# Kernel optimization log

Measured on AMD Instinct MI355X. Metric: run time of the kernel, lower is better.

Reference implementation:

```python
import jax, jax.numpy as jnp
import numpy as np
from jax import lax

B, N, D = 64, 499, 256          # batch, nodes(=seq_len), emb_size
NUM_P, NUM_Q, NUM_C = 10000, 2000, 10


def _seg_softmax(e, dst, n):
    # e: [E,H] edge scores, segment softmax over destination node
    m = jax.ops.segment_max(e, dst, num_segments=n)
    ex = jnp.exp(e - m[dst])
    s = jax.ops.segment_sum(ex, dst, num_segments=n)
    return ex / s[dst]


def gat_conv(x, src, dst, W, a_src, a_dst, b, concat):
    # x: [B,n,Fin], W: [Fin,H*Fo], a_src/a_dst: [H,Fo], b: [H*Fo] or [Fo]
    Bn, n, _ = x.shape
    H, Fo = a_src.shape
    h = (x @ W).reshape(Bn, n, H, Fo)
    es = jnp.einsum('bnhf,hf->bnh', h, a_src)
    ed = jnp.einsum('bnhf,hf->bnh', h, a_dst)
    e = jax.nn.leaky_relu(es[:, src] + ed[:, dst], 0.2)   # [B,E,H]
    alpha = jax.vmap(lambda eb: _seg_softmax(eb, dst, n))(e)
    msg = alpha[..., None] * h[:, src]                    # [B,E,H,Fo]
    out = jax.vmap(lambda mb: jax.ops.segment_sum(mb, dst, num_segments=n))(msg)
    out = out.reshape(Bn, n, H * Fo) if concat else out.mean(axis=2)
    return out + b


def lstm(xs, W_ih, W_hh, b_ih, b_hh):
    # xs: [B,S,I]; torch gate order i,f,g,o
    Bn = xs.shape[0]
    Hd = W_hh.shape[1]

    def step(carry, xt):
        h, c = carry
        g = xt @ W_ih.T + b_ih + h @ W_hh.T + b_hh
        i, f, gg, o = jnp.split(g, 4, axis=-1)
        c = jax.nn.sigmoid(f) * c + jax.nn.sigmoid(i) * jnp.tanh(gg)
        h = jax.nn.sigmoid(o) * jnp.tanh(c)
        return (h, c), h

    init = (jnp.zeros((Bn, Hd), xs.dtype), jnp.zeros((Bn, Hd), xs.dtype))
    _, hs = lax.scan(step, init, xs.transpose(1, 0, 2))
    return hs.transpose(1, 0, 2)


def _edges():
    # genr_edge_index(true_length-1=498): chain over nodes 0..497, then
    # PyG GATConv removes self-loops and adds them back for all 499 nodes.
    L = N - 1
    src, dst = [], []
    for i in range(L):
        for j in (i - 1, i + 1):
            if 0 <= j < L:
                src.append(i)
                dst.append(j)
    src += list(range(N))
    dst += list(range(N))
    return np.array(src, np.int32), np.array(dst, np.int32)


def setup_inputs() -> dict:
    key = jax.random.key(0)
    ks = jax.random.split(key, 30)
    f32 = jnp.float32

    def nrm(k, shape, s=0.05):
        return jax.random.normal(k, shape, dtype=f32) * s

    src, dst = _edges()
    inp = {
        'true_length': jnp.full((B,), N, dtype=jnp.int32),
        'p': jax.random.randint(ks[0], (B, N), 0, NUM_P + 1, dtype=jnp.int32),
        'q': jax.random.randint(ks[1], (B, N), 0, NUM_Q + 1, dtype=jnp.int32),
        'r': jax.random.randint(ks[2], (B, N), 0, 2, dtype=jnp.int32),
        'aff': jax.random.randint(ks[3], (B, N), 0, NUM_C + 1, dtype=jnp.int32),
        'q_next': jax.random.randint(ks[4], (B, N), 0, NUM_Q + 1, dtype=jnp.int32),
        'p_next': jax.random.randint(ks[5], (B, N), 0, NUM_P + 1, dtype=jnp.int32),
        'src': jnp.asarray(src),
        'dst': jnp.asarray(dst),
        'emb_p': nrm(ks[6], (NUM_P + 1, D), 1.0),
        'emb_q': nrm(ks[7], (NUM_Q + 1, D), 1.0),
        'emb_r': nrm(ks[8], (2, D), 1.0),
        'emb_aff': nrm(ks[9], (NUM_C + 1, D), 1.0),
        'W_affcat': nrm(ks[10], (2 * D, D)),
        'b_affcat': nrm(ks[11], (D,)),
        'W_g1': nrm(ks[12], (D, 8 * 128)),
        'a_src1': nrm(ks[13], (8, 128)),
        'a_dst1': nrm(ks[14], (8, 128)),
        'b_g1': nrm(ks[15], (8 * 128,)),
        'W_g2': nrm(ks[16], (8 * 128, D)),
        'a_src2': nrm(ks[17], (1, D)),
        'a_dst2': nrm(ks[18], (1, D)),
        'b_g2': nrm(ks[19], (D,)),
        'W_ih': nrm(ks[20], (4 * D, 4 * D)),
        'W_hh': nrm(ks[21], (4 * D, D)),
        'b_ih': nrm(ks[22], (4 * D,)),
        'b_hh': nrm(ks[23], (4 * D,)),
        'W_out': nrm(ks[24], (3 * D, 1)),
        'b_out': nrm(ks[25], (1,)),
    }
    return inp


def reference(true_length, p, q, r, aff, q_next, p_next, src, dst,
              emb_p, emb_q, emb_r, emb_aff, W_affcat, b_affcat,
              W_g1, a_src1, a_dst1, b_g1, W_g2, a_src2, a_dst2, b_g2,
              W_ih, W_hh, b_ih, b_hh, W_out, b_out):
    # eval mode: all dropouts are identity
    p_emb = emb_p[p]            # [B,N,D]
    q_emb = emb_q[q]
    r_emb = emb_r[r]
    qn_emb = emb_q[q_next]
    pn_emb = emb_p[p_next]
    aff_emb = emb_aff[aff]

    x = jnp.concatenate([p_emb, aff_emb], axis=-1) @ W_affcat + b_affcat
    x = jax.nn.elu(gat_conv(x, src, dst, W_g1, a_src1, a_dst1, b_g1, True))
    x = gat_conv(x, src, dst, W_g2, a_src2, a_dst2, b_g2, False)   # [B,N,D]

    seq = jnp.concatenate([p_emb, q_emb, r_emb, x], axis=-1)       # [B,N,4D]
    h = lstm(seq, W_ih, W_hh, b_ih, b_hh)                          # [B,N,D]
    y = jnp.concatenate([h, qn_emb, pn_emb], axis=-1) @ W_out + b_out
    return jax.nn.sigmoid(y)
```

## Files before the change

### kernel.cpp

```cpp
#include <hip/hip_runtime.h>
#include <hip/hip_bf16.h>

typedef unsigned int u32;
typedef unsigned short u16;

#define MTOT 31936
#define NN 499
#define BB 64

__device__ __forceinline__ float lo16(u32 u){ return __uint_as_float(u << 16); }
__device__ __forceinline__ float hi16(u32 u){ return __uint_as_float(u & 0xffff0000u); }
__device__ __forceinline__ float bf2f(u16 u){ return __uint_as_float(((u32)u) << 16); }
__device__ __forceinline__ u16 f2bf(float f){
  u32 x = __float_as_uint(f);
  u32 r = (x + 0x7fffu + ((x >> 16) & 1u)) >> 16;
  return (u16)r;
}
__device__ __forceinline__ float sigf(float x){ return 1.f / (1.f + __expf(-x)); }
__device__ __forceinline__ float tanh_(float x){ return 2.f * sigf(2.f * x) - 1.f; }
__device__ __forceinline__ float wred(float v){
  #pragma unroll
  for (int off = 32; off; off >>= 1) v += __shfl_down(v, off, 64);
  return v;
}

typedef __attribute__((ext_vector_type(2))) __bf16 bf16x2;
#if __has_builtin(__builtin_amdgcn_fdot2_f32_bf16)
__device__ __forceinline__ float dot2bf(u32 w, u32 h, float acc){
  union { u32 u; bf16x2 v; } uw, uh;
  uw.u = w; uh.u = h;
  return __builtin_amdgcn_fdot2_f32_bf16(uw.v, uh.v, acc, false);
}
#else
__device__ __forceinline__ float dot2bf(u32 w, u32 h, float acc){
  return acc + lo16(w) * lo16(h) + hi16(w) * hi16(h);
}
#endif

#if __has_builtin(__builtin_amdgcn_cvt_pk_bf16_f32)
__device__ __forceinline__ u32 pk2bf(float a, float b){
  union { bf16x2 v; u32 u; } r;
  r.v = __builtin_amdgcn_cvt_pk_bf16_f32(a, b);
  return r.u;
}
#else
__device__ __forceinline__ u32 pk2bf(float a, float b){
  return (u32)f2bf(a) | ((u32)f2bf(b) << 16);
}
#endif

typedef __attribute__((ext_vector_type(8))) short bfrag8;
typedef __attribute__((ext_vector_type(4))) float f4_t;
union FragU { uint4 u; bfrag8 s; };

__device__ __forceinline__ f4_t mfma16(FragU a, FragU b, f4_t c){
  return __builtin_amdgcn_mfma_f32_16x16x32_bf16(a.s, b.s, c, 0, 0, 0);
}

template <typename AL>
__device__ __forceinline__ void gemm_core2(int K32, const uint4* __restrict__ Bpack,
                                           f4_t (&acc)[4][2], AL aload){
  __shared__ __align__(16) uint4 As[2][256];
  const int tid = threadIdx.x;
  const int wave = tid >> 6, lane = tid & 63;
  const uint4* Bp0 = Bpack + ((size_t)(blockIdx.y * 8 + wave * 2) * K32) * 64 + lane;
  const uint4* Bp1 = Bp0 + (size_t)K32 * 64;
  int buf = 0;
  for (int kt = 0; kt < K32; kt++){
    FragU b0, b1;
    b0.u = Bp0[kt * 64];
    b1.u = Bp1[kt * 64];
    As[buf][tid] = aload(kt);
    __syncthreads();
    FragU a0, a1, a2, a3;
    a0.u = As[buf][lane];
    a1.u = As[buf][64 + lane];
    a2.u = As[buf][128 + lane];
    a3.u = As[buf][192 + lane];
    acc[0][0] = mfma16(a0, b0, acc[0][0]); acc[0][1] = mfma16(a0, b1, acc[0][1]);
    acc[1][0] = mfma16(a1, b0, acc[1][0]); acc[1][1] = mfma16(a1, b1, acc[1][1]);
    acc[2][0] = mfma16(a2, b0, acc[2][0]); acc[2][1] = mfma16(a2, b1, acc[2][1]);
    acc[3][0] = mfma16(a3, b0, acc[3][0]); acc[3][1] = mfma16(a3, b1, acc[3][1]);
    buf ^= 1;
  }
}

__global__ __launch_bounds__(256) void k_packB(const float* __restrict__ W, u16* __restrict__ out,
                                               int K, int N, int trans){
  int c = blockIdx.x * 256 + threadIdx.x;
  int K32 = K >> 5;
  int total = (N >> 4) * K32 * 64;
  if (c >= total) return;
  int l = c & 63;
  int rem = c >> 6;
  int kt = rem % K32, nt = rem / K32;
  int n = nt * 16 + (l & 15);
  int kb = kt * 32 + (l >> 4) * 8;
  u32 ov[4];
  #pragma unroll
  for (int j2 = 0; j2 < 4; j2++){
    int k = kb + j2 * 2;
    float f0 = trans ? W[(size_t)n * K + k]     : W[(size_t)k * N + n];
    float f1 = trans ? W[(size_t)n * K + k + 1] : W[(size_t)(k + 1) * N + n];
    ov[j2] = pk2bf(f0, f1);
  }
  uint4 o; o.x = ov[0]; o.y = ov[1]; o.z = ov[2]; o.w = ov[3];
  *(uint4*)(out + (size_t)c * 8) = o;
}

__global__ void k_csr(const int* __restrict__ src, const int* __restrict__ dst, int E,
                      int* __restrict__ deg, int* __restrict__ insrc){
  int tid = threadIdx.x;
  for (int i = tid; i < NN; i += 256) deg[i] = 0;
  for (int i = tid; i < NN * 4; i += 256) insrc[i] = 0;
  __syncthreads();
  for (int e = tid; e < E; e += 256){
    int d = dst[e];
    int slot = atomicAdd(&deg[d], 1);
    if (slot < 4) insrc[d * 4 + slot] = src[e];
  }
}

__global__ void k_packwhh(const float* __restrict__ Whh, uint4* __restrict__ whh4){
  int idx = blockIdx.x * 256 + threadIdx.x;
  int j = idx & 1023, kc = idx >> 10;
  const float* w = Whh + (size_t)j * 256 + kc * 8;
  float4 w0 = *(const float4*)w;
  float4 w1 = *(const float4*)(w + 4);
  uint4 o;
  o.x = pk2bf(w0.x, w0.y);
  o.y = pk2bf(w0.z, w0.w);
  o.z = pk2bf(w1.x, w1.y);
  o.w = pk2bf(w1.z, w1.w);
  whh4[kc * 1024 + j] = o;
}

__global__ __launch_bounds__(256) void k_affcat_m(
    const float* __restrict__ emb_p, const float* __restrict__ emb_aff,
    const int* __restrict__ p, const int* __restrict__ aff,
    const uint4* __restrict__ Bpack, const float* __restrict__ bias, float* __restrict__ C){
  const int tid = threadIdx.x;
  const int mBase = blockIdx.x * 64, nBase = blockIdx.y * 128;
  const int ls = tid & 63;
  const int gm = mBase + (tid >> 6) * 16 + (ls & 15);
  const int kqoff = (ls >> 4) * 8;
  const float* rp = emb_p + (size_t)p[gm] * 256 + kqoff;
  const float* ra = emb_aff + (size_t)aff[gm] * 256 + kqoff;
  f4_t acc[4][2] = {};
  gemm_core2(16, Bpack, acc, [&](int kt) -> uint4 {
    int kb = kt * 32;
    const float* s = (kb < 256) ? (rp + kb) : (ra + kb - 256);
    float4 v0 = *(const float4*)s;
    float4 v1 = *(const float4*)(s + 4);
    uint4 o; o.x = pk2bf(v0.x, v0.y); o.y = pk2bf(v0.z, v0.w);
    o.z = pk2bf(v1.x, v1.y); o.w = pk2bf(v1.z, v1.w);
    return o;
  });
  const int wave = tid >> 6, lane = tid & 63;
  const int rb = (lane >> 4) << 2;
  const int cbase = nBase + wave * 32 + (lane & 15);
  float b0 = bias[cbase], b1 = bias[cbase + 16];
  #pragma unroll
  for (int i = 0; i < 4; i++)
    #pragma unroll
    for (int r = 0; r < 4; r++){
      int row = mBase + i * 16 + rb + r;
      C[(size_t)row * 256 + cbase]      = acc[i][0][r] + b0;
      C[(size_t)row * 256 + cbase + 16] = acc[i][1][r] + b1;
    }
}

__global__ __launch_bounds__(256) void k_h1_m(const float* __restrict__ A,
                                              const uint4* __restrict__ Bpack,
                                              u16* __restrict__ Cb){
  const int tid = threadIdx.x;
  const int mBase = blockIdx.x * 64, nBase = blockIdx.y * 128;
  const int ls = tid & 63;
  const int gm = mBase + (tid >> 6) * 16 + (ls & 15);
  const float* ra = A + (size_t)gm * 256 + (ls >> 4) * 8;
  f4_t acc[4][2] = {};
  gemm_core2(8, Bpack, acc, [&](int kt) -> uint4 {
    const float* s = ra + kt * 32;
    float4 v0 = *(const float4*)s;
    float4 v1 = *(const float4*)(s + 4);
    uint4 o; o.x = pk2bf(v0.x, v0.y); o.y = pk2bf(v0.z, v0.w);
    o.z = pk2bf(v1.x, v1.y); o.w = pk2bf(v1.z, v1.w);
    return o;
  });
  const int wave = tid >> 6, lane = tid & 63;
  const int rb = (lane >> 4) << 2;
  const int cbase = nBase + wave * 32 + (lane & 15);
  #pragma unroll
  for (int i = 0; i < 4; i++)
    #pragma unroll
    for (int r = 0; r < 4; r++){
      int row = mBase + i * 16 + rb + r;
      Cb[(size_t)row * 1024 + cbase]      = f2bf(acc[i][0][r]);
      Cb[(size_t)row * 1024 + cbase + 16] = f2bf(acc[i][1][r]);
    }
}

__global__ __launch_bounds__(256) void k_h2_m(const u16* __restrict__ A,
                                              const uint4* __restrict__ Bpack,
                                              float* __restrict__ C){
  const int tid = threadIdx.x;
  const int mBase = blockIdx.x * 64, nBase = blockIdx.y * 128;
  const int ls = tid & 63;
  const int gm = mBase + (tid >> 6) * 16 + (ls & 15);
  const u16* ra = A + (size_t)gm * 1024 + (ls >> 4) * 8;
  f4_t acc[4][2] = {};
  gemm_core2(32, Bpack, acc, [&](int kt) -> uint4 {
    return *(const uint4*)(ra + kt * 32);
  });
  const int wave = tid >> 6, lane = tid & 63;
  const int rb = (lane >> 4) << 2;
  const int cbase = nBase + wave * 32 + (lane & 15);
  #pragma unroll
  for (int i = 0; i < 4; i++)
    #pragma unroll
    for (int r = 0; r < 4; r++){
      int row = mBase + i * 16 + rb + r;
      C[(size_t)row * 256 + cbase]      = acc[i][0][r];
      C[(size_t)row * 256 + cbase + 16] = acc[i][1][r];
    }
}

__global__ __launch_bounds__(256) void k_gates_m(
    const float* __restrict__ emb_p, const float* __restrict__ emb_q, const float* __restrict__ emb_r,
    const int* __restrict__ p, const int* __restrict__ q, const int* __restrict__ r,
    const float* __restrict__ x2, const uint4* __restrict__ Bpack,
    const float* __restrict__ bih, const float* __restrict__ bhh, u16* __restrict__ Cb){
  const int tid = threadIdx.x;
  const int mBase = blockIdx.x * 64, nBase = blockIdx.y * 128;
  const int ls = tid & 63;
  const int gm = mBase + (tid >> 6) * 16 + (ls & 15);
  const int kqoff = (ls >> 4) * 8;
  const float* s0 = emb_p + (size_t)p[gm] * 256 + kqoff;
  const float* s1 = emb_q + (size_t)q[gm] * 256 + kqoff;
  const float* s2 = emb_r + (size_t)r[gm] * 256 + kqoff;
  const float* s3 = x2 + (size_t)gm * 256 + kqoff;
  f4_t acc[4][2] = {};
  gemm_core2(32, Bpack, acc, [&](int kt) -> uint4 {
    int kb = kt * 32;
    int seg = kb >> 8, ko = kb & 255;
    const float* s = (seg == 0) ? s0 : ((seg == 1) ? s1 : ((seg == 2) ? s2 : s3));
    float4 v0 = *(const float4*)(s + ko);
    float4 v1 = *(const float4*)(s + ko + 4);
    uint4 o; o.x = pk2bf(v0.x, v0.y); o.y = pk2bf(v0.z, v0.w);
    o.z = pk2bf(v1.x, v1.y); o.w = pk2bf(v1.z, v1.w);
    return o;
  });
  const int wave = tid >> 6, lane = tid & 63;
  const int rb = (lane >> 4) << 2;
  const int cbase = nBase + wave * 32 + (lane & 15);
  float b0 = bih[cbase] + bhh[cbase];
  float b1 = bih[cbase + 16] + bhh[cbase + 16];
  #pragma unroll
  for (int i = 0; i < 4; i++)
    #pragma unroll
    for (int r2 = 0; r2 < 4; r2++){
      int row = mBase + i * 16 + rb + r2;
      Cb[(size_t)row * 1024 + cbase]      = f2bf(acc[i][0][r2] + b0);
      Cb[(size_t)row * 1024 + cbase + 16] = f2bf(acc[i][1][r2] + b1);
    }
}

__global__ __launch_bounds__(256) void k_esed(
    const u16* __restrict__ hb, const float* __restrict__ hf,
    const float* __restrict__ asrc, const float* __restrict__ adst,
    float* __restrict__ es, float* __restrict__ ed, int Hm1, int Fo){
  int w = blockIdx.x * 4 + (threadIdx.x >> 6);
  int lane = threadIdx.x & 63;
  int h = w & Hm1;
  size_t base = (size_t)w * Fo;
  float s = 0.f, d = 0.f;
  for (int f = lane; f < Fo; f += 64){
    float hv = hb ? bf2f(hb[base + f]) : hf[base + f];
    s += hv * asrc[h * Fo + f];
    d += hv * adst[h * Fo + f];
  }
  s = wred(s); d = wred(d);
  if (!lane){ es[w] = s; ed[w] = d; }
}

__global__ __launch_bounds__(256) void k_gatagg(
    const u16* __restrict__ hb, const float* __restrict__ hf,
    const float* __restrict__ es, const float* __restrict__ ed,
    const int* __restrict__ deg, const int* __restrict__ insrc,
    const float* __restrict__ bias, u16* __restrict__ outb, float* __restrict__ outf,
    int H, int foShift, int HFo, int do_elu){
  int m = blockIdx.x;
  int b = m / NN;
  int n = m - b * NN;
  int dg = deg[n];
  int s0 = insrc[n * 4 + 0];
  int s1 = insrc[n * 4 + 1];
  int s2 = insrc[n * 4 + 2];
  int rowBase = b * NN;
  for (int c = threadIdx.x; c < HFo; c += 256){
    int h = c >> foShift;
    float edv = ed[(size_t)m * H + h];
    float sc0 = es[(size_t)(rowBase + s0) * H + h] + edv;
    sc0 = (sc0 >= 0.f) ? sc0 : 0.2f * sc0;
    float sc1 = 0.f, sc2 = 0.f, mx = sc0;
    if (dg > 1){ sc1 = es[(size_t)(rowBase + s1) * H + h] + edv; sc1 = (sc1 >= 0.f) ? sc1 : 0.2f * sc1; mx = fmaxf(mx, sc1); }
    if (dg > 2){ sc2 = es[(size_t)(rowBase + s2) * H + h] + edv; sc2 = (sc2 >= 0.f) ? sc2 : 0.2f * sc2; mx = fmaxf(mx, sc2); }
    float e0 = __expf(sc0 - mx), e1 = 0.f, e2 = 0.f;
    if (dg > 1) e1 = __expf(sc1 - mx);
    if (dg > 2) e2 = __expf(sc2 - mx);
    float inv = 1.f / (e0 + e1 + e2);
    size_t c0 = (size_t)(rowBase + s0) * HFo + c;
    float acc = e0 * (hb ? bf2f(hb[c0]) : hf[c0]);
    if (dg > 1){ size_t c1 = (size_t)(rowBase + s1) * HFo + c; acc += e1 * (hb ? bf2f(hb[c1]) : hf[c1]); }
    if (dg > 2){ size_t c2 = (size_t)(rowBase + s2) * HFo + c; acc += e2 * (hb ? bf2f(hb[c2]) : hf[c2]); }
    acc *= inv;
    float o = acc + bias[c];
    if (do_elu) o = (o > 0.f) ? o : (__expf(o) - 1.f);
    if (outb) outb[(size_t)m * HFo + c] = f2bf(o);
    else      outf[(size_t)m * HFo + c] = o;
  }
}

#define KREG 18
#define KLDS 9
__global__ __launch_bounds__(1024)
__attribute__((amdgpu_waves_per_eu(1, 4)))
void k_lstm(const u16* __restrict__ gates,
            const uint4* __restrict__ whh4,
            float* __restrict__ h_all){
  __shared__ __align__(16) uint4 wlds[KLDS][1024];
  __shared__ __align__(16) u32 h2_lds[128];
  __shared__ float dots[1024];
  const int b = blockIdx.x, t = threadIdx.x;
  const int lane = t & 63;
  float c = 0.f;
  if (t < 128) h2_lds[t] = 0;
  uint4 wreg[KREG];
  #pragma unroll
  for (int kc = 0; kc < KREG; kc++) wreg[kc] = whh4[kc * 1024 + t];
  #pragma unroll
  for (int kc = 0; kc < KLDS; kc++) wlds[kc][t] = whh4[(KREG + kc) * 1024 + t];
  __syncthreads();
  const u16* gb = gates + (size_t)b * NN * 1024;
  const uint4* wbase = whh4 + (KREG + KLDS) * 1024 + t;
  for (int n = 0; n < NN; n++){
    uint4 hvec = *(const uint4*)&h2_lds[(lane & 31) * 4];
    float acc0 = bf2f(gb[(size_t)n * 1024 + t]);
    float acc1 = 0.f;
    #pragma unroll
    for (int i = 0; i < 32 - KREG - KLDS; i++){
      const int kc = KREG + KLDS + i;
      uint4 w = wbase[i * 1024];
      u32 hx = (u32)__builtin_amdgcn_readlane((int)hvec.x, kc);
      u32 hy = (u32)__builtin_amdgcn_readlane((int)hvec.y, kc);
      u32 hz = (u32)__builtin_amdgcn_readlane((int)hvec.z, kc);
      u32 hw = (u32)__builtin_amdgcn_readlane((int)hvec.w, kc);
      acc0 = dot2bf(w.x, hx, acc0);
      acc1 = dot2bf(w.y, hy, acc1);
      acc0 = dot2bf(w.z, hz, acc0);
      acc1 = dot2bf(w.w, hw, acc1);
    }
    #pragma unroll
    for (int i = 0; i < KLDS; i++){
      const int kc = KREG + i;
      uint4 w = wlds[i][t];
      u32 hx = (u32)__builtin_amdgcn_readlane((int)hvec.x, kc);
      u32 hy = (u32)__builtin_amdgcn_readlane((int)hvec.y, kc);
      u32 hz = (u32)__builtin_amdgcn_readlane((int)hvec.z, kc);
      u32 hw = (u32)__builtin_amdgcn_readlane((int)hvec.w, kc);
      acc0 = dot2bf(w.x, hx, acc0);
      acc1 = dot2bf(w.y, hy, acc1);
      acc0 = dot2bf(w.z, hz, acc0);
      acc1 = dot2bf(w.w, hw, acc1);
    }
    #pragma unroll
    for (int kc = 0; kc < KREG; kc++){
      uint4 w = wreg[kc];
      u32 hx = (u32)__builtin_amdgcn_readlane((int)hvec.x, kc);
      u32 hy = (u32)__builtin_amdgcn_readlane((int)hvec.y, kc);
      u32 hz = (u32)__builtin_amdgcn_readlane((int)hvec.z, kc);
      u32 hw = (u32)__builtin_amdgcn_readlane((int)hvec.w, kc);
      acc0 = dot2bf(w.x, hx, acc0);
      acc1 = dot2bf(w.y, hy, acc1);
      acc0 = dot2bf(w.z, hz, acc0);
      acc1 = dot2bf(w.w, hw, acc1);
    }
    dots[t] = acc0 + acc1;
    __syncthreads();
    if (t < 256){
      float ai = dots[t], af = dots[256 + t], ag = dots[512 + t], ao = dots[768 + t];
      c = sigf(af) * c + sigf(ai) * tanh_(ag);
      float h = sigf(ao) * tanh_(c);
      h_all[((size_t)b * NN + n) * 256 + t] = h;
      ((u16*)h2_lds)[t] = f2bf(h);
    }
    __syncthreads();
  }
}

__global__ __launch_bounds__(256) void k_out(const float* __restrict__ h_all,
    const float* __restrict__ emb_q, const float* __restrict__ emb_p,
    const int* __restrict__ qn, const int* __restrict__ pn,
    const float* __restrict__ Wo, const float* __restrict__ bo, float* __restrict__ y){
  int m = blockIdx.x * 4 + (threadIdx.x >> 6);
  int lane = threadIdx.x & 63;
  const float* hr = h_all + (size_t)m * 256;
  const float* rq = emb_q + (size_t)qn[m] * 256;
  const float* rp = emb_p + (size_t)pn[m] * 256;
  float acc = 0.f;
  #pragma unroll
  for (int f = 0; f < 256; f += 64){
    int d = f + lane;
    acc += hr[d] * Wo[d];
    acc += rq[d] * Wo[256 + d];
    acc += rp[d] * Wo[512 + d];
  }
  acc = wred(acc);
  if (!lane) y[m] = sigf(acc + bo[0]);
}

extern "C" void kernel_launch(void* const* d_in, const int* in_sizes, int n_in,
                              void* d_out, int out_size, void* d_ws, size_t ws_size,
                              hipStream_t stream){
  (void)n_in; (void)out_size; (void)ws_size;
  const int* p    = (const int*)d_in[1];
  const int* q    = (const int*)d_in[2];
  const int* r    = (const int*)d_in[3];
  const int* aff  = (const int*)d_in[4];
  const int* qn   = (const int*)d_in[5];
  const int* pn   = (const int*)d_in[6];
  const int* src  = (const int*)d_in[7];
  const int* dst  = (const int*)d_in[8];
  const float* emb_p  = (const float*)d_in[9];
  const float* emb_q  = (const float*)d_in[10];
  const float* emb_r  = (const float*)d_in[11];
  const float* emb_aff= (const float*)d_in[12];
  const float* W_aff  = (const float*)d_in[13];
  const float* b_aff  = (const float*)d_in[14];
  const float* W_g1   = (const float*)d_in[15];
  const float* a_s1   = (const float*)d_in[16];
  const float* a_d1   = (const float*)d_in[17];
  const float* b_g1   = (const float*)d_in[18];
  const float* W_g2   = (const float*)d_in[19];
  const float* a_s2   = (const float*)d_in[20];
  const float* a_d2   = (const float*)d_in[21];
  const float* b_g2   = (const float*)d_in[22];
  const float* W_ih   = (const float*)d_in[23];
  const float* W_hh   = (const float*)d_in[24];
  const float* b_ih   = (const float*)d_in[25];
  const float* b_hh   = (const float*)d_in[26];
  const float* W_out  = (const float*)d_in[27];
  const float* b_out  = (const float*)d_in[28];
  const int E = in_sizes[7];

  char* ws = (char*)d_ws;
  size_t off = 0;
  auto alloc = [&](size_t bytes){ size_t ret = off; off += (bytes + 255) & ~(size_t)255; return ret; };
  size_t o_bigA = alloc((size_t)MTOT * 1024 * 2);
  size_t o_bigB = alloc((size_t)MTOT * 1024 * 2);
  size_t o_buf3 = alloc((size_t)MTOT * 256 * 4);
  size_t o_es1 = alloc((size_t)MTOT * 8 * 4);
  size_t o_ed1 = alloc((size_t)MTOT * 8 * 4);
  size_t o_es2 = alloc((size_t)MTOT * 4);
  size_t o_ed2 = alloc((size_t)MTOT * 4);
  size_t o_whh = alloc((size_t)32 * 1024 * 16);
  size_t o_deg = alloc(512 * 4);
  size_t o_ins = alloc((size_t)NN * 4 * 4);
  size_t o_bpih  = alloc((size_t)131072 * 16);
  size_t o_bpg1  = alloc((size_t)32768 * 16);
  size_t o_bpg2  = alloc((size_t)32768 * 16);
  size_t o_bpaff = alloc((size_t)16384 * 16);

  u16*   h1    = (u16*)(ws + o_bigA);
  u16*   gates = (u16*)(ws + o_bigA);
  u16*   g1out = (u16*)(ws + o_bigB);
  float* x2    = (float*)(ws + o_bigB);
  float* x0    = (float*)(ws + o_buf3);
  float* h2    = (float*)(ws + o_buf3);
  float* h_all = (float*)(ws + o_buf3);
  float* es1   = (float*)(ws + o_es1);
  float* ed1   = (float*)(ws + o_ed1);
  float* es2   = (float*)(ws + o_es2);
  float* ed2   = (float*)(ws + o_ed2);
  uint4* whh4  = (uint4*)(ws + o_whh);
  int*   degp  = (int*)(ws + o_deg);
  int*   insp  = (int*)(ws + o_ins);
  u16*   bpih  = (u16*)(ws + o_bpih);
  u16*   bpg1  = (u16*)(ws + o_bpg1);
  u16*   bpg2  = (u16*)(ws + o_bpg2);
  u16*   bpaff = (u16*)(ws + o_bpaff);

  k_csr<<<1, 256, 0, stream>>>(src, dst, E, degp, insp);
  k_packwhh<<<128, 256, 0, stream>>>(W_hh, whh4);
  k_packB<<<512, 256, 0, stream>>>(W_ih, bpih, 1024, 1024, 1);
  k_packB<<<128, 256, 0, stream>>>(W_g1, bpg1, 256, 1024, 0);
  k_packB<<<128, 256, 0, stream>>>(W_g2, bpg2, 1024, 256, 0);
  k_packB<<<64, 256, 0, stream>>>(W_aff, bpaff, 512, 256, 0);

  k_affcat_m<<<dim3(NN, 2), 256, 0, stream>>>(emb_p, emb_aff, p, aff,
                                              (const uint4*)bpaff, b_aff, x0);
  k_h1_m<<<dim3(NN, 8), 256, 0, stream>>>(x0, (const uint4*)bpg1, h1);
  k_esed<<<(MTOT * 8) / 4, 256, 0, stream>>>(h1, nullptr, a_s1, a_d1, es1, ed1, 7, 128);
  k_gatagg<<<MTOT, 256, 0, stream>>>(h1, nullptr, es1, ed1, degp, insp, b_g1,
                                     g1out, nullptr, 8, 7, 1024, 1);
  k_h2_m<<<dim3(NN, 2), 256, 0, stream>>>(g1out, (const uint4*)bpg2, h2);
  k_esed<<<MTOT / 4, 256, 0, stream>>>(nullptr, h2, a_s2, a_d2, es2, ed2, 0, 256);
  k_gatagg<<<MTOT, 256, 0, stream>>>(nullptr, h2, es2, ed2, degp, insp, b_g2,
                                     nullptr, x2, 1, 8, 256, 0);
  k_gates_m<<<dim3(NN, 8), 256, 0, stream>>>(emb_p, emb_q, emb_r, p, q, r, x2,
                                             (const uint4*)bpih, b_ih, b_hh, gates);
  k_lstm<<<BB, 1024, 0, stream>>>(gates, whh4, h_all);
  k_out<<<MTOT / 4, 256, 0, stream>>>(h_all, emb_q, emb_p, qn, pn, W_out, b_out, (float*)d_out);
}
```

Measured before the change: 1.797 ms.

## Interleave LSTM gate rows per wave to replace LDS gate exchange with shuffles

Repacks W_hh so that each wave holds the i, f, g and o rows for the same 16 hidden units. The gate nonlinearities can then be combined with intra-wave shuffles instead of writing dots to LDS and hitting a second block barrier. h is double-buffered so each step needs only one __syncthreads, and the next step's gate input is prefetched into a register to hide its global load latency. Every lane now computes the cell update redundantly, and only one lane in four writes the result.

After: 2.012 ms. 1.12x slower.

```diff
diff --git a/kernel.cpp b/kernel.cpp
--- a/kernel.cpp
+++ b/kernel.cpp
@@ -123,7 +123,8 @@
 
 __global__ void k_packwhh(const float* __restrict__ Whh, uint4* __restrict__ whh4){
   int idx = blockIdx.x * 256 + threadIdx.x;
-  int j = idx & 1023, kc = idx >> 10;
+  int t = idx & 1023, kc = idx >> 10;
+  int j = ((t >> 4) & 3) * 256 + (t >> 6) * 16 + (t & 15);
   const float* w = Whh + (size_t)j * 256 + kc * 8;
   float4 w0 = *(const float4*)w;
   float4 w1 = *(const float4*)(w + 4);
@@ -132,7 +133,7 @@
   o.y = pk2bf(w0.z, w0.w);
   o.z = pk2bf(w1.x, w1.y);
   o.w = pk2bf(w1.z, w1.w);
-  whh4[kc * 1024 + j] = o;
+  whh4[kc * 1024 + t] = o;
 }
 
 __global__ __launch_bounds__(256) void k_affcat_m(
@@ -329,23 +330,27 @@
             const uint4* __restrict__ whh4,
             float* __restrict__ h_all){
   __shared__ __align__(16) uint4 wlds[KLDS][1024];
-  __shared__ __align__(16) u32 h2_lds[128];
-  __shared__ float dots[1024];
+  __shared__ __align__(16) u32 h2b[2][128];
   const int b = blockIdx.x, t = threadIdx.x;
-  const int lane = t & 63;
+  const int l = t & 63, wv = t >> 6;
+  const int uu = l & 15, g = l >> 4;
+  const int u = wv * 16 + uu;
   float c = 0.f;
-  if (t < 128) h2_lds[t] = 0;
+  if (t < 256) ((u32*)h2b)[t] = 0;
   uint4 wreg[KREG];
   #pragma unroll
   for (int kc = 0; kc < KREG; kc++) wreg[kc] = whh4[kc * 1024 + t];
   #pragma unroll
   for (int kc = 0; kc < KLDS; kc++) wlds[kc][t] = whh4[(KREG + kc) * 1024 + t];
   __syncthreads();
-  const u16* gb = gates + (size_t)b * NN * 1024;
+  const u16* gb = gates + (size_t)b * NN * 1024 + (g * 256 + u);
   const uint4* wbase = whh4 + (KREG + KLDS) * 1024 + t;
+  u16 gcur = gb[0];
   for (int n = 0; n < NN; n++){
-    uint4 hvec = *(const uint4*)&h2_lds[(lane & 31) * 4];
-    float acc0 = bf2f(gb[(size_t)n * 1024 + t]);
+    uint4 hvec = *(const uint4*)&h2b[n & 1][(l & 31) * 4];
+    int nn = (n + 1 < NN) ? (n + 1) : n;
+    u16 gnext = gb[(size_t)nn * 1024];
+    float acc0 = bf2f(gcur);
     float acc1 = 0.f;
     #pragma unroll
     for (int i = 0; i < 32 - KREG - KLDS; i++){
@@ -385,15 +390,18 @@
       acc0 = dot2bf(w.z, hz, acc0);
       acc1 = dot2bf(w.w, hw, acc1);
     }
-    dots[t] = acc0 + acc1;
-    __syncthreads();
-    if (t < 256){
-      float ai = dots[t], af = dots[256 + t], ag = dots[512 + t], ao = dots[768 + t];
-      c = sigf(af) * c + sigf(ai) * tanh_(ag);
-      float h = sigf(ao) * tanh_(c);
-      h_all[((size_t)b * NN + n) * 256 + t] = h;
-      ((u16*)h2_lds)[t] = f2bf(h);
-    }
+    float dot = acc0 + acc1;
+    float ai = __shfl(dot, uu, 64);
+    float af = __shfl(dot, 16 + uu, 64);
+    float ag = __shfl(dot, 32 + uu, 64);
+    float ao = __shfl(dot, 48 + uu, 64);
+    c = sigf(af) * c + sigf(ai) * tanh_(ag);
+    float h = sigf(ao) * tanh_(c);
+    if (g == 0){
+      h_all[((size_t)b * NN + n) * 256 + u] = h;
+      ((u16*)h2b[(n + 1) & 1])[u] = f2bf(h);
+    }
+    gcur = gnext;
     __syncthreads();
   }
 }
```
